# Kernel optimization log

Measured on AMD Instinct MI355X. Metric: run time of the kernel, lower is better.

Reference implementation:

```python
import jax, jax.numpy as jnp
import numpy as np

B, S, D = 16, 1024, 512
N_LAYERS = 3


def setup_inputs() -> dict:
    key = jax.random.key(0)
    ks = jax.random.split(key, 8)
    sc = 0.02  # small init scale keeps gates in a sane range
    return {
        "inputs": jax.random.normal(ks[0], (B, S, D), jnp.float32),
        "h0": jax.random.normal(ks[1], (N_LAYERS, B, D), jnp.float32),
        # GRU params, PyTorch layout: gates ordered (r, z, n), weight [3D, D]
        "w_ih": jax.random.normal(ks[2], (N_LAYERS, 3 * D, D), jnp.float32) * sc,
        "w_hh": jax.random.normal(ks[3], (N_LAYERS, 3 * D, D), jnp.float32) * sc,
        "b_ih": jnp.zeros((N_LAYERS, 3 * D), jnp.float32),
        "b_hh": jnp.zeros((N_LAYERS, 3 * D), jnp.float32),
        "ln0_g": jnp.ones((D,), jnp.float32),
        "ln0_b": jnp.zeros((D,), jnp.float32),
        "ln1_g": jnp.ones((D,), jnp.float32),
        "ln1_b": jnp.zeros((D,), jnp.float32),
        "w1": jax.random.normal(ks[4], (D, 4 * D), jnp.float32) * sc,
        "b1": jnp.zeros((4 * D,), jnp.float32),
        "w2": jax.random.normal(ks[5], (4 * D, D), jnp.float32) * sc,
        "b2": jnp.zeros((D,), jnp.float32),
    }


def _layer_norm(x, g, b, eps=1e-5):
    mu = jnp.mean(x, axis=-1, keepdims=True)
    var = jnp.var(x, axis=-1, keepdims=True)
    return (x - mu) * jax.lax.rsqrt(var + eps) * g + b


def _gru_stack(x, h0, w_ih, w_hh, b_ih, b_hh):
    # x: [S, B, D] time-major; PyTorch GRU math, gate order (r, z, n).
    for l in range(N_LAYERS):
        # precompute input projections for all timesteps (batched GEMM)
        gi = jnp.einsum('sbd,gd->sbg', x, w_ih[l]) + b_ih[l]  # [S, B, 3D]
        w_hh_l_T = w_hh[l].T
        b_hh_l = b_hh[l]

        def step(h, gi_t):
            gh = h @ w_hh_l_T + b_hh_l                       # [B, 3D]
            i_r, i_z, i_n = jnp.split(gi_t, 3, axis=-1)
            h_r, h_z, h_n = jnp.split(gh, 3, axis=-1)
            r = jax.nn.sigmoid(i_r + h_r)
            z = jax.nn.sigmoid(i_z + h_z)
            n = jnp.tanh(i_n + r * h_n)
            h_new = (1.0 - z) * n + z * h
            return h_new, h_new

        _, x = jax.lax.scan(step, h0[l], gi)                 # x: [S, B, D]
    return x


def reference(inputs, h0, w_ih, w_hh, b_ih, b_hh,
              ln0_g, ln0_b, ln1_g, ln1_b, w1, b1, w2, b2):
    # inputs: [B, S, D] -> time-major [S, B, D]
    x = _layer_norm(jnp.transpose(inputs, (1, 0, 2)), ln0_g, ln0_b)
    h = _gru_stack(x, h0, w_ih, w_hh, b_ih, b_hh)            # [S, B, D]
    out = inputs + jnp.transpose(h, (1, 0, 2))               # residual 1 (dropout=identity, eval)
    y = _layer_norm(out, ln1_g, ln1_b)
    ffn = jax.nn.gelu(y @ w1 + b1, approximate=False) @ w2 + b2
    return out + ffn                                          # residual 2
```

## Files before the change

### kernel.cpp

```cpp
#include <hip/hip_runtime.h>
#include <hip/hip_bf16.h>

typedef unsigned short u16;
typedef unsigned int   u32;
typedef unsigned long long u64;
typedef __attribute__((ext_vector_type(8))) short short8;
typedef __attribute__((ext_vector_type(4))) float f32x4;

#define WDMAX (1 << 17)

__device__ __forceinline__ float bf2f(u16 u) {
  union { u32 i; float f; } v; v.i = ((u32)u) << 16; return v.f;
}
__device__ __forceinline__ u16 f2bf(float f) {
  union { float f; u32 i; } v; v.f = f;
  return (u16)((v.i + 0x7FFFu + ((v.i >> 16) & 1u)) >> 16);
}

typedef const __attribute__((address_space(1))) u32* gas_t;
typedef __attribute__((address_space(3)))       u32* las_t;
__device__ __forceinline__ void gld16(const void* g, void* l) {
  __builtin_amdgcn_global_load_lds((gas_t)g, (las_t)l, 16, 0, 0);
}

#define WG_BARRIER() asm volatile("s_waitcnt lgkmcnt(0)\n\ts_barrier" ::: "memory")

__global__ __launch_bounds__(256) void cast_kernel(const float* __restrict__ src,
                                                   u16* __restrict__ dst, int n) {
  int i = (blockIdx.x * 256 + threadIdx.x) * 4;
  if (i >= n) return;
  float4 v = *(const float4*)(src + i);
  uint2 o;
  o.x = (u32)f2bf(v.x) | ((u32)f2bf(v.y) << 16);
  o.y = (u32)f2bf(v.z) | ((u32)f2bf(v.w) << 16);
  *(uint2*)(dst + i) = o;
}

__global__ __launch_bounds__(256) void tcast_kernel(const float* __restrict__ src,
                                                    u16* __restrict__ dst, int R, int C) {
  __shared__ u16 tile[32][33];
  int c0 = blockIdx.x * 32, r0 = blockIdx.y * 32;
  for (int dy = threadIdx.y; dy < 32; dy += 8)
    tile[dy][threadIdx.x] = f2bf(src[(size_t)(r0 + dy) * C + c0 + threadIdx.x]);
  __syncthreads();
  for (int dy = threadIdx.y; dy < 32; dy += 8)
    dst[(size_t)(c0 + dy) * R + r0 + threadIdx.x] = tile[threadIdx.x][dy];
}

__global__ __launch_bounds__(256) void hprep_kernel(const float* __restrict__ h0,
                                                    u64* __restrict__ hbuf) {
  int l = blockIdx.x;
  const float* h = h0 + l * 8192;
  u64* buf = hbuf + (size_t)l * 2 * 4096;
  for (int idx = threadIdx.x; idx < 4096; idx += 256) {
    int row = idx >> 8, wl = idx & 255;
    int d0 = wl * 2;
    u64 p0 = f2bf(h[row * 512 + d0]);
    u64 p1 = f2bf(h[row * 512 + d0 + 1]);
    buf[idx] = p0 | (p1 << 32);
  }
}

__global__ __launch_bounds__(256) void ln0_kernel(const float* __restrict__ in,
                                                  const float* __restrict__ g,
                                                  const float* __restrict__ be,
                                                  u16* __restrict__ xout) {
  int m = blockIdx.x;
  int b = m >> 10, s = m & 1023;
  int i = threadIdx.x * 2;
  float2 v = *(const float2*)(in + (size_t)m * 512 + i);
  float sum = v.x + v.y, sq = v.x * v.x + v.y * v.y;
  for (int o = 32; o > 0; o >>= 1) { sum += __shfl_down(sum, o); sq += __shfl_down(sq, o); }
  __shared__ float red[10];
  int w = threadIdx.x >> 6, lane = threadIdx.x & 63;
  if (!lane) { red[w] = sum; red[w + 4] = sq; }
  __syncthreads();
  if (threadIdx.x == 0) {
    sum = red[0] + red[1] + red[2] + red[3];
    sq  = red[4] + red[5] + red[6] + red[7];
    float mu = sum * (1.f / 512.f), var = sq * (1.f / 512.f) - mu * mu;
    red[8] = mu; red[9] = rsqrtf(var + 1e-5f);
  }
  __syncthreads();
  float mu = red[8], rs = red[9];
  u32 o0 = (u32)f2bf((v.x - mu) * rs * g[i] + be[i]) |
           ((u32)f2bf((v.y - mu) * rs * g[i + 1] + be[i + 1]) << 16);
  *(u32*)(xout + (size_t)(s * 16 + b) * 512 + i) = o0;
}

__global__ __launch_bounds__(256) void resid_ln1_kernel(const float* __restrict__ in,
                                                        const u16* __restrict__ hrec,
                                                        const float* __restrict__ g,
                                                        const float* __restrict__ be,
                                                        float* __restrict__ outf,
                                                        u16* __restrict__ y) {
  int m = blockIdx.x;
  int b = m >> 10, s = m & 1023;
  int i = threadIdx.x * 2;
  float2 v = *(const float2*)(in + (size_t)m * 512 + i);
  u32 hu = *(const u32*)(hrec + (size_t)(s * 16 + b) * 512 + i);
  v.x += bf2f((u16)(hu & 0xffff));
  v.y += bf2f((u16)(hu >> 16));
  *(float2*)(outf + (size_t)m * 512 + i) = v;
  float sum = v.x + v.y, sq = v.x * v.x + v.y * v.y;
  for (int o = 32; o > 0; o >>= 1) { sum += __shfl_down(sum, o); sq += __shfl_down(sq, o); }
  __shared__ float red[10];
  int w = threadIdx.x >> 6, lane = threadIdx.x & 63;
  if (!lane) { red[w] = sum; red[w + 4] = sq; }
  __syncthreads();
  if (threadIdx.x == 0) {
    sum = red[0] + red[1] + red[2] + red[3];
    sq  = red[4] + red[5] + red[6] + red[7];
    float mu = sum * (1.f / 512.f), var = sq * (1.f / 512.f) - mu * mu;
    red[8] = mu; red[9] = rsqrtf(var + 1e-5f);
  }
  __syncthreads();
  float mu = red[8], rs = red[9];
  u32 o0 = (u32)f2bf((v.x - mu) * rs * g[i] + be[i]) |
           ((u32)f2bf((v.y - mu) * rs * g[i + 1] + be[i + 1]) << 16);
  *(u32*)(y + (size_t)m * 512 + i) = o0;
}

template <int EPI>
__global__ __launch_bounds__(256, 2)
void gemm_bt(const u16* __restrict__ A, const u16* __restrict__ Bt,
             void* __restrict__ Out, const float* __restrict__ bias,
             const float* __restrict__ resid, int M, int N, int K) {
  __shared__ u16 As[128 * 64];
  __shared__ u16 Bs[128 * 64];
  const int bn = blockIdx.x, bm = blockIdx.y;
  const int tid = threadIdx.x;
  const int w = tid >> 6, lane = tid & 63;
  const int wr = w >> 1, wc = w & 1;
  const int col = lane & 15, kg = lane >> 4;
  const int l8 = lane >> 3, l7 = lane & 7;
  f32x4 acc[4][4];
#pragma unroll
  for (int i = 0; i < 4; ++i)
#pragma unroll
    for (int j = 0; j < 4; ++j) acc[i][j] = (f32x4){0.f, 0.f, 0.f, 0.f};

  for (int k0 = 0; k0 < K; k0 += 64) {
    __syncthreads();
#pragma unroll
    for (int i = 0; i < 4; ++i) {
      int q = w * 4 + i;
      int row = q * 8 + l8;
      int cswz = (l7 * 16) ^ ((row & 7) << 4);
      gld16((const char*)A + ((size_t)(bm * 128 + row) * K + k0) * 2 + cswz,
            (char*)As + q * 1024);
      gld16((const char*)Bt + ((size_t)(bn * 128 + row) * K + k0) * 2 + cswz,
            (char*)Bs + q * 1024);
    }
    asm volatile("s_waitcnt vmcnt(0)" ::: "memory");
    __syncthreads();
#pragma unroll
    for (int kc = 0; kc < 2; ++kc) {
      short8 af[4], bfr[4];
      int cb = kc * 64 + kg * 16;
#pragma unroll
      for (int mi = 0; mi < 4; ++mi) {
        int r = wr * 64 + mi * 16 + col;
        af[mi] = *(const short8*)((const char*)As + r * 128 + (cb ^ ((r & 7) << 4)));
      }
#pragma unroll
      for (int ni = 0; ni < 4; ++ni) {
        int r = wc * 64 + ni * 16 + col;
        bfr[ni] = *(const short8*)((const char*)Bs + r * 128 + (cb ^ ((r & 7) << 4)));
      }
#pragma unroll
      for (int mi = 0; mi < 4; ++mi)
#pragma unroll
        for (int ni = 0; ni < 4; ++ni)
          acc[mi][ni] = __builtin_amdgcn_mfma_f32_16x16x32_bf16(af[mi], bfr[ni], acc[mi][ni], 0, 0, 0);
    }
  }
#pragma unroll
  for (int ni = 0; ni < 4; ++ni) {
    int gn = bn * 128 + wc * 64 + ni * 16 + col;
    float bv = bias ? bias[gn] : 0.f;
#pragma unroll
    for (int mi = 0; mi < 4; ++mi) {
      int gmb = bm * 128 + wr * 64 + mi * 16 + kg * 4;
#pragma unroll
      for (int j = 0; j < 4; ++j) {
        float v = acc[mi][ni][j] + bv;
        size_t idx = (size_t)(gmb + j) * N + gn;
        if (EPI == 0) {
          ((u16*)Out)[idx] = f2bf(v);
        } else if (EPI == 1) {
          float gel = 0.5f * v * (1.f + erff(v * 0.7071067811865476f));
          ((u16*)Out)[idx] = f2bf(gel);
        } else {
          ((float*)Out)[idx] = v + resid[idx];
        }
      }
    }
  }
}

__device__ __forceinline__ void gather_poll(const u64* __restrict__ plane, u32 want,
                                            int w, int lane, u16* __restrict__ lds) {
  const u64 TM = 0xFFFF0000FFFF0000ULL;
  const u64 ex = ((u64)want << 16) | ((u64)want << 48);
  u64 v[16];
#pragma unroll
  for (int r = 0; r < 4; ++r)
#pragma unroll
    for (int q = 0; q < 4; ++q)
      v[r * 4 + q] = __hip_atomic_load(plane + (size_t)(w * 4 + r) * 256 + lane * 4 + q,
                                       __ATOMIC_RELAXED, __HIP_MEMORY_SCOPE_AGENT);
  for (int wd = 0; wd < WDMAX; ++wd) {
    bool ok = true;
#pragma unroll
    for (int i = 0; i < 16; ++i) ok &= ((v[i] ^ ex) & TM) == 0;
    if (ok) break;
    __builtin_amdgcn_s_sleep(1);
#pragma unroll
    for (int i = 0; i < 16; ++i)
      if (((v[i] ^ ex) & TM) != 0)
        v[i] = __hip_atomic_load(plane + (size_t)(w * 4 + (i >> 2)) * 256 + lane * 4 + (i & 3),
                                 __ATOMIC_RELAXED, __HIP_MEMORY_SCOPE_AGENT);
  }
#pragma unroll
  for (int r = 0; r < 4; ++r) {
    int row = w * 4 + r;
    uint4 pk;
    pk.x = ((u32)v[r * 4 + 0] & 0xFFFFu) | ((u32)(v[r * 4 + 0] >> 32) << 16);
    pk.y = ((u32)v[r * 4 + 1] & 0xFFFFu) | ((u32)(v[r * 4 + 1] >> 32) << 16);
    pk.z = ((u32)v[r * 4 + 2] & 0xFFFFu) | ((u32)(v[r * 4 + 2] >> 32) << 16);
    pk.w = ((u32)v[r * 4 + 3] & 0xFFFFu) | ((u32)(v[r * 4 + 3] >> 32) << 16);
    *(uint4*)((char*)lds + row * 1024 + ((lane * 16) ^ ((row & 7) << 4))) = pk;
  }
}

__global__ __launch_bounds__(256, 1)
void rec3_kernel(const u16* __restrict__ gib, const u16* __restrict__ whhb,
                 const u16* __restrict__ wihb, const float* __restrict__ bih,
                 const float* __restrict__ bhh, const float* __restrict__ h0,
                 u64* __restrict__ hpl, u64* __restrict__ xr,
                 u64* __restrict__ gip, u16* __restrict__ xout) {
  const int res = blockIdx.x & 7, grp = blockIdx.x >> 3;
  if (res > 4) return;
  __shared__ u16 hs[16 * 512];
  const int tid = threadIdx.x;
  const int w = tid >> 6, lane = tid & 63;
  const int col = lane & 15, kg = lane >> 4;
  const u64 TM = 0xFFFF0000FFFF0000ULL;

  if (res >= 3) {
    const int l = res - 2, k = grp;
    const int d = k * 64 + w * 16 + col;
    const u16* wih = wihb + (size_t)l * 1536 * 512;
    short8 wi0[16], wi1[16], wi2[16];
    {
      const u16* r0 = wih + (size_t)(0 * 512 + d) * 512;
      const u16* r1 = wih + (size_t)(1 * 512 + d) * 512;
      const u16* r2 = wih + (size_t)(2 * 512 + d) * 512;
#pragma unroll
      for (int kc = 0; kc < 16; ++kc) {
        wi0[kc] = *(const short8*)(r0 + kc * 32 + kg * 8);
        wi1[kc] = *(const short8*)(r1 + kc * 32 + kg * 8);
        wi2[kc] = *(const short8*)(r2 + kc * 32 + kg * 8);
      }
    }
    const float bi0 = bih[l * 1536 + d], bi1 = bih[l * 1536 + 512 + d],
                bi2 = bih[l * 1536 + 1024 + d];
    const u64* upx = xr + (size_t)(l - 1) * 8 * 4096;
    u64* gout = gip + (size_t)(l - 1) * 4 * 12288;
    const u64* hpc = hpl + (size_t)l * 2 * 4096;
    u64 bpv = 0;
    u64 xv[16];
    {
      const u64* pl = upx + 1 * 4096;
#pragma unroll
      for (int r = 0; r < 4; ++r)
#pragma unroll
        for (int q = 0; q < 4; ++q)
          xv[r * 4 + q] = __hip_atomic_load(pl + (size_t)(w * 4 + r) * 256 + lane * 4 + q,
                                            __ATOMIC_RELAXED, __HIP_MEMORY_SCOPE_AGENT);
    }
    for (int t = 1; t <= 1024; ++t) {
      const u64* pl = upx + (size_t)(t & 7) * 4096;
      const u64 ex = ((u64)t << 16) | ((u64)t << 48);
      for (int wd = 0; wd < WDMAX; ++wd) {
        bool ok = true;
#pragma unroll
        for (int i = 0; i < 16; ++i) ok &= ((xv[i] ^ ex) & TM) == 0;
        if (ok) break;
        __builtin_amdgcn_s_sleep(1);
#pragma unroll
        for (int r = 0; r < 4; ++r)
#pragma unroll
          for (int q = 0; q < 4; ++q)
            if (((xv[r * 4 + q] ^ ex) & TM) != 0)
              xv[r * 4 + q] = __hip_atomic_load(pl + (size_t)(w * 4 + r) * 256 + lane * 4 + q,
                                                __ATOMIC_RELAXED, __HIP_MEMORY_SCOPE_AGENT);
      }
      {
#pragma unroll
        for (int r = 0; r < 4; ++r) {
          int row = w * 4 + r;
          uint4 pk;
          pk.x = ((u32)xv[r*4+0] & 0xFFFFu) | ((u32)(xv[r*4+0] >> 32) << 16);
          pk.y = ((u32)xv[r*4+1] & 0xFFFFu) | ((u32)(xv[r*4+1] >> 32) << 16);
          pk.z = ((u32)xv[r*4+2] & 0xFFFFu) | ((u32)(xv[r*4+2] >> 32) << 16);
          pk.w = ((u32)xv[r*4+3] & 0xFFFFu) | ((u32)(xv[r*4+3] >> 32) << 16);
          *(uint4*)((char*)hs + row * 1024 + ((lane * 16) ^ ((row & 7) << 4))) = pk;
        }
      }
      WG_BARRIER();
      f32x4 ar = {0.f, 0.f, 0.f, 0.f}, az = ar, an = ar;
#pragma unroll
      for (int kc = 0; kc < 16; ++kc) {
        int cb = kc * 64 + kg * 16;
        short8 a = *(const short8*)((const char*)hs + col * 1024 + (cb ^ ((col & 7) << 4)));
        ar = __builtin_amdgcn_mfma_f32_16x16x32_bf16(a, wi0[kc], ar, 0, 0, 0);
        az = __builtin_amdgcn_mfma_f32_16x16x32_bf16(a, wi1[kc], az, 0, 0, 0);
        an = __builtin_amdgcn_mfma_f32_16x16x32_bf16(a, wi2[kc], an, 0, 0, 0);
      }
      if (t > 4) {
        u32 need = (u32)(t - 4);
        u32 ctag = (u32)(bpv >> 16) & 0xFFFFu;
        for (int wd = 0; wd < WDMAX && ctag < need; ++wd) {
          __builtin_amdgcn_s_sleep(8);
          bpv = __hip_atomic_load(hpc + (size_t)(need & 1) * 4096 + k * 32,
                                  __ATOMIC_RELAXED, __HIP_MEMORY_SCOPE_AGENT);
          ctag = (u32)(bpv >> 16) & 0xFFFFu;
        }
      }
      {
        const u32 tgl = (u32)t << 16;
        u64* slot = gout + (size_t)(t & 3) * 12288 + (size_t)k * 1536;
#pragma unroll
        for (int g = 0; g < 3; ++g) {
          f32x4 a = (g == 0) ? ar : ((g == 1) ? az : an);
          float bg = (g == 0) ? bi0 : ((g == 1) ? bi1 : bi2);
#pragma unroll
          for (int jh = 0; jh < 2; ++jh) {
            u32 lo = (u32)f2bf(a[2 * jh] + bg) | tgl;
            u32 hi = (u32)f2bf(a[2 * jh + 1] + bg) | tgl;
            __hip_atomic_store(slot + (size_t)(g * 64 + w * 16 + col) * 8 + kg * 2 + jh,
                               (u64)lo | ((u64)hi << 32),
                               __ATOMIC_RELAXED, __HIP_MEMORY_SCOPE_AGENT);
          }
        }
      }
      if (t >= 4)
        bpv = __hip_atomic_load(hpc + (size_t)((t - 3) & 1) * 4096 + k * 32,
                                __ATOMIC_RELAXED, __HIP_MEMORY_SCOPE_AGENT);
      if (t < 1024) {
        const u64* np = upx + (size_t)((t + 1) & 7) * 4096;
#pragma unroll
        for (int r = 0; r < 4; ++r)
#pragma unroll
          for (int q = 0; q < 4; ++q)
            xv[r * 4 + q] = __hip_atomic_load(np + (size_t)(w * 4 + r) * 256 + lane * 4 + q,
                                              __ATOMIC_RELAXED, __HIP_MEMORY_SCOPE_AGENT);
      }
      WG_BARRIER();
    }
    return;
  }

  const int l = res, blk = grp;
  const int d = blk * 64 + w * 16 + col;
  const u16* whh = whhb + (size_t)l * 1536 * 512;
  short8 wh0[16], wh1[16], wh2[16];
  {
    const u16* r0 = whh + (size_t)(0 * 512 + d) * 512;
    const u16* r1 = whh + (size_t)(1 * 512 + d) * 512;
    const u16* r2 = whh + (size_t)(2 * 512 + d) * 512;
#pragma unroll
    for (int kc = 0; kc < 16; ++kc) {
      wh0[kc] = *(const short8*)(r0 + kc * 32 + kg * 8);
      wh1[kc] = *(const short8*)(r1 + kc * 32 + kg * 8);
      wh2[kc] = *(const short8*)(r2 + kc * 32 + kg * 8);
    }
  }
  const float bh0 = bhh[l * 1536 + d], bh1 = bhh[l * 1536 + 512 + d],
              bh2 = bhh[l * 1536 + 1024 + d];
  float hprev[4];
#pragma unroll
  for (int j = 0; j < 4; ++j) hprev[j] = h0[l * 8192 + (kg * 4 + j) * 512 + d];

  u64* ownp = hpl + (size_t)l * 2 * 4096;
  u64* dnx = xr + (size_t)l * 8 * 4096;
  const u64* gin = gip + (size_t)(l - 1) * 4 * 12288;
  const u64* gchk = gip + (size_t)l * 4 * 12288;
  const bool ev = !(col & 1);
  u64 bp8 = 0;
  u64 gv[6] = {0, 0, 0, 0, 0, 0};

  for (int t = 1; t <= 1024; ++t) {
    float gir[3][4];
    if (l == 0) {
#pragma unroll
      for (int gte = 0; gte < 3; ++gte)
#pragma unroll
        for (int j = 0; j < 4; ++j)
          gir[gte][j] = bf2f(gib[((size_t)(t - 1) * 16 + kg * 4 + j) * 1536 + gte * 512 + d]);
    }
    gather_poll(ownp + (size_t)((t - 1) & 1) * 4096, (u32)(t - 1), w, lane, hs);
    if (l > 0) {
      const u64* gs = gin + (size_t)(t & 3) * 12288 + (size_t)blk * 1536;
      const u64 exg = ((u64)t << 16) | ((u64)t << 48);
      for (int wd = 0; wd < WDMAX; ++wd) {
        bool ok = true;
#pragma unroll
        for (int i = 0; i < 6; ++i) ok &= ((gv[i] ^ exg) & TM) == 0;
        if (ok) break;
        __builtin_amdgcn_s_sleep(1);
#pragma unroll
        for (int g = 0; g < 3; ++g)
#pragma unroll
          for (int jh = 0; jh < 2; ++jh)
            if (((gv[g * 2 + jh] ^ exg) & TM) != 0)
              gv[g * 2 + jh] = __hip_atomic_load(gs + (size_t)(g * 64 + w * 16 + col) * 8 + kg * 2 + jh,
                                                 __ATOMIC_RELAXED, __HIP_MEMORY_SCOPE_AGENT);
      }
#pragma unroll
      for (int g = 0; g < 3; ++g)
#pragma unroll
        for (int jh = 0; jh < 2; ++jh) {
          gir[g][2 * jh]     = bf2f((u16)gv[g * 2 + jh]);
          gir[g][2 * jh + 1] = bf2f((u16)(gv[g * 2 + jh] >> 32));
        }
    }
    WG_BARRIER();
    f32x4 ar = {0.f, 0.f, 0.f, 0.f}, az = ar, an = ar;
#pragma unroll
    for (int kc = 0; kc < 16; ++kc) {
      int cb = kc * 64 + kg * 16;
      short8 a = *(const short8*)((const char*)hs + col * 1024 + (cb ^ ((col & 7) << 4)));
      ar = __builtin_amdgcn_mfma_f32_16x16x32_bf16(a, wh0[kc], ar, 0, 0, 0);
      az = __builtin_amdgcn_mfma_f32_16x16x32_bf16(a, wh1[kc], az, 0, 0, 0);
      an = __builtin_amdgcn_mfma_f32_16x16x32_bf16(a, wh2[kc], an, 0, 0, 0);
    }
    u32 po[4];
#pragma unroll
    for (int j = 0; j < 4; ++j) {
      float rg = 1.f / (1.f + expf(-(gir[0][j] + ar[j] + bh0)));
      float zg = 1.f / (1.f + expf(-(gir[1][j] + az[j] + bh1)));
      float ng = tanhf(gir[2][j] + rg * (an[j] + bh2));
      float hn = (1.f - zg) * ng + zg * hprev[j];
      hprev[j] = hn;
      po[j] = (u32)f2bf(hn);
    }
    {
      const u32 tg = (u32)t << 16;
      u32 pn[4];
#pragma unroll
      for (int j = 0; j < 4; ++j) pn[j] = (u32)__shfl_xor((int)po[j], 1);
      int j0 = ev ? 0 : 2;
      u64 wd_[2]; int wi_[2];
#pragma unroll
      for (int jj = 0; jj < 2; ++jj) {
        int j = j0 + jj;
        u32 lo = (ev ? po[j] : pn[j]) | tg;
        u32 hi = (ev ? pn[j] : po[j]) | tg;
        int row = kg * 4 + j;
        wd_[jj] = (u64)lo | ((u64)hi << 32);
        wi_[jj] = row * 256 + blk * 32 + w * 8 + (col >> 1);
      }
      u64* op = ownp + (size_t)(t & 1) * 4096;
#pragma unroll
      for (int jj = 0; jj < 2; ++jj)
        __hip_atomic_store(op + wi_[jj], wd_[jj], __ATOMIC_RELAXED, __HIP_MEMORY_SCOPE_AGENT);

      if (l < 2) {
        if (t > 8) {
          u32 need = (u32)(t - 8);
          for (int wd = 0; wd < WDMAX; ++wd) {
            u32 tg8 = (lane < 8) ? (u32)((bp8 >> 16) & 0xFFFFu) : 0xFFFFu;
            if (__all(tg8 >= need)) break;
            __builtin_amdgcn_s_sleep(8);
            if (lane < 8)
              bp8 = __hip_atomic_load(gchk + (size_t)(need & 3) * 12288 + (size_t)lane * 1536,
                                      __ATOMIC_RELAXED, __HIP_MEMORY_SCOPE_AGENT);
          }
        }
        u64* xp = dnx + (size_t)(t & 7) * 4096;
#pragma unroll
        for (int jj = 0; jj < 2; ++jj)
          __hip_atomic_store(xp + wi_[jj], wd_[jj], __ATOMIC_RELAXED, __HIP_MEMORY_SCOPE_AGENT);
        if (t >= 8 && lane < 8)
          bp8 = __hip_atomic_load(gchk + (size_t)((t - 7) & 3) * 12288 + (size_t)lane * 1536,
                                  __ATOMIC_RELAXED, __HIP_MEMORY_SCOPE_AGENT);
      } else {
        u32 pr[4], qr[4];
#pragma unroll
        for (int j = 0; j < 4; ++j) {
          pr[j] = ev ? (po[j] | (pn[j] << 16)) : (pn[j] | (po[j] << 16));
          qr[j] = (u32)__shfl_xor((int)pr[j], 2);
        }
        int jx = col & 3;
        u64 raw = ((col & 2) == 0) ? ((u64)pr[jx] | ((u64)qr[jx] << 32))
                                   : ((u64)qr[jx] | ((u64)pr[jx] << 32));
        int row = kg * 4 + jx;
        *(u64*)(xout + ((size_t)(t - 1) * 16 + row) * 512 + blk * 64 + w * 16 + (col & ~3)) = raw;
      }
    }
    if (l > 0 && t < 1024) {
      const u64* gs2 = gin + (size_t)((t + 1) & 3) * 12288 + (size_t)blk * 1536;
#pragma unroll
      for (int g = 0; g < 3; ++g)
#pragma unroll
        for (int jh = 0; jh < 2; ++jh)
          gv[g * 2 + jh] = __hip_atomic_load(gs2 + (size_t)(g * 64 + w * 16 + col) * 8 + kg * 2 + jh,
                                             __ATOMIC_RELAXED, __HIP_MEMORY_SCOPE_AGENT);
    }
    WG_BARRIER();
  }
}

extern "C" void kernel_launch(void* const* d_in, const int* in_sizes, int n_in,
                              void* d_out, int out_size, void* d_ws, size_t ws_size,
                              hipStream_t stream) {
  const float* inp = (const float*)d_in[0];
  const float* h0  = (const float*)d_in[1];
  const float* wih = (const float*)d_in[2];
  const float* whh = (const float*)d_in[3];
  const float* bih = (const float*)d_in[4];
  const float* bhh = (const float*)d_in[5];
  const float* g0  = (const float*)d_in[6];
  const float* be0 = (const float*)d_in[7];
  const float* g1  = (const float*)d_in[8];
  const float* be1 = (const float*)d_in[9];
  const float* w1  = (const float*)d_in[10];
  const float* b1  = (const float*)d_in[11];
  const float* w2  = (const float*)d_in[12];
  const float* b2  = (const float*)d_in[13];
  float* out = (float*)d_out;

  char* p = (char*)d_ws;
  auto alloc = [&](size_t bytes) {
    char* r = p;
    p += (bytes + 255) & ~(size_t)255;
    return r;
  };
  u16* xa    = (u16*)alloc(16384ull * 512 * 2);
  u16* xb    = (u16*)alloc(16384ull * 512 * 2);
  u16* gib   = (u16*)alloc(16384ull * 1536 * 2);
  u16* mid   = (u16*)alloc(16384ull * 2048 * 2);
  float* outf = (float*)alloc(16384ull * 512 * 4);
  u16* wihb  = (u16*)alloc(3ull * 1536 * 512 * 2);
  u16* whhb  = (u16*)alloc(3ull * 1536 * 512 * 2);
  u16* w1t   = (u16*)alloc(2048ull * 512 * 2);
  u16* w2t   = (u16*)alloc(512ull * 2048 * 2);
  u64* hbuf  = (u64*)alloc(3ull * 2 * 4096 * 8);
  u64* xr    = (u64*)alloc(2ull * 8 * 4096 * 8);
  u64* gip   = (u64*)alloc(2ull * 4 * 12288 * 8);

  (void)hipMemsetAsync(hbuf, 0, 3ull * 2 * 4096 * 8, stream);
  (void)hipMemsetAsync(xr,   0, 2ull * 8 * 4096 * 8, stream);
  (void)hipMemsetAsync(gip,  0, 2ull * 4 * 12288 * 8, stream);
  cast_kernel<<<(3 * 1536 * 512) / 1024, 256, 0, stream>>>(wih, wihb, 3 * 1536 * 512);
  cast_kernel<<<(3 * 1536 * 512) / 1024, 256, 0, stream>>>(whh, whhb, 3 * 1536 * 512);
  hprep_kernel<<<3, 256, 0, stream>>>(h0, hbuf);
  tcast_kernel<<<dim3(2048 / 32, 512 / 32), dim3(32, 8), 0, stream>>>(w1, w1t, 512, 2048);
  tcast_kernel<<<dim3(512 / 32, 2048 / 32), dim3(32, 8), 0, stream>>>(w2, w2t, 2048, 512);
  ln0_kernel<<<16384, 256, 0, stream>>>(inp, g0, be0, xa);

  gemm_bt<0><<<dim3(12, 128), 256, 0, stream>>>(xa, wihb, (void*)gib, bih, nullptr,
                                                16384, 1536, 512);
  rec3_kernel<<<64, 256, 0, stream>>>(gib, whhb, wihb, bih, bhh, h0, hbuf, xr, gip, xb);

  resid_ln1_kernel<<<16384, 256, 0, stream>>>(inp, xb, g1, be1, outf, xa);
  gemm_bt<1><<<dim3(16, 128), 256, 0, stream>>>(xa, w1t, (void*)mid, b1, nullptr,
                                                16384, 2048, 512);
  gemm_bt<2><<<dim3(4, 128), 256, 0, stream>>>(mid, w2t, (void*)out, b2, outf,
                                               16384, 512, 2048);
}
```

Before: 4.982 ms.

## Fuse layer-0 input projection into persistent recurrence kernel with deeper ring buffers

```diff
diff --git a/kernel.cpp b/kernel.cpp
--- a/kernel.cpp
+++ b/kernel.cpp
@@ -24,6 +24,7 @@
 }
 
 #define WG_BARRIER() asm volatile("s_waitcnt lgkmcnt(0)\n\ts_barrier" ::: "memory")
+#define C_FENCE() asm volatile("" ::: "memory")
 
 __global__ __launch_bounds__(256) void cast_kernel(const float* __restrict__ src,
                                                    u16* __restrict__ dst, int n) {
@@ -186,9 +187,7 @@
       for (int j = 0; j < 4; ++j) {
         float v = acc[mi][ni][j] + bv;
         size_t idx = (size_t)(gmb + j) * N + gn;
-        if (EPI == 0) {
-          ((u16*)Out)[idx] = f2bf(v);
-        } else if (EPI == 1) {
+        if (EPI == 1) {
           float gel = 0.5f * v * (1.f + erff(v * 0.7071067811865476f));
           ((u16*)Out)[idx] = f2bf(gel);
         } else {
@@ -235,21 +234,21 @@
 }
 
 __global__ __launch_bounds__(256, 1)
-void rec3_kernel(const u16* __restrict__ gib, const u16* __restrict__ whhb,
+void rec3_kernel(const u16* __restrict__ xa, const u16* __restrict__ whhb,
                  const u16* __restrict__ wihb, const float* __restrict__ bih,
                  const float* __restrict__ bhh, const float* __restrict__ h0,
                  u64* __restrict__ hpl, u64* __restrict__ xr,
                  u64* __restrict__ gip, u16* __restrict__ xout) {
   const int res = blockIdx.x & 7, grp = blockIdx.x >> 3;
-  if (res > 4) return;
-  __shared__ u16 hs[16 * 512];
+  if (res > 5) return;
+  __shared__ u16 hs[2][16 * 512];
   const int tid = threadIdx.x;
   const int w = tid >> 6, lane = tid & 63;
   const int col = lane & 15, kg = lane >> 4;
   const u64 TM = 0xFFFF0000FFFF0000ULL;
 
   if (res >= 3) {
-    const int l = res - 2, k = grp;
+    const int l = res - 3, k = grp;
     const int d = k * 64 + w * 16 + col;
     const u16* wih = wihb + (size_t)l * 1536 * 512;
     short8 wi0[16], wi1[16], wi2[16];
@@ -266,12 +265,12 @@
     }
     const float bi0 = bih[l * 1536 + d], bi1 = bih[l * 1536 + 512 + d],
                 bi2 = bih[l * 1536 + 1024 + d];
-    const u64* upx = xr + (size_t)(l - 1) * 8 * 4096;
-    u64* gout = gip + (size_t)(l - 1) * 4 * 12288;
+    const u64* upx = (l > 0) ? (xr + (size_t)(l - 1) * 16 * 4096) : nullptr;
+    u64* gout = gip + (size_t)l * 8 * 12288;
     const u64* hpc = hpl + (size_t)l * 2 * 4096;
-    u64 bpv = 0;
+    u64 pv = 0;
     u64 xv[16];
-    {
+    if (l > 0) {
       const u64* pl = upx + 1 * 4096;
 #pragma unroll
       for (int r = 0; r < 4; ++r)
@@ -281,23 +280,33 @@
                                             __ATOMIC_RELAXED, __HIP_MEMORY_SCOPE_AGENT);
     }
     for (int t = 1; t <= 1024; ++t) {
-      const u64* pl = upx + (size_t)(t & 7) * 4096;
-      const u64 ex = ((u64)t << 16) | ((u64)t << 48);
-      for (int wd = 0; wd < WDMAX; ++wd) {
-        bool ok = true;
-#pragma unroll
-        for (int i = 0; i < 16; ++i) ok &= ((xv[i] ^ ex) & TM) == 0;
-        if (ok) break;
-        __builtin_amdgcn_s_sleep(1);
-#pragma unroll
-        for (int r = 0; r < 4; ++r)
-#pragma unroll
-          for (int q = 0; q < 4; ++q)
-            if (((xv[r * 4 + q] ^ ex) & TM) != 0)
-              xv[r * 4 + q] = __hip_atomic_load(pl + (size_t)(w * 4 + r) * 256 + lane * 4 + q,
-                                                __ATOMIC_RELAXED, __HIP_MEMORY_SCOPE_AGENT);
-      }
-      {
+      u16* hsb = hs[t & 1];
+      if (l == 0) {
+        const char* src = (const char*)(xa + (size_t)(t - 1) * 8192);
+        const u32 lo = (u32)(lane * 16);
+#pragma unroll
+        for (int r = 0; r < 4; ++r) {
+          int row = w * 4 + r;
+          *(uint4*)((char*)hsb + row * 1024 + (lo ^ (u32)((row & 7) << 4))) =
+              *(const uint4*)(src + row * 1024 + lo);
+        }
+      } else {
+        const u64* pl = upx + (size_t)(t & 15) * 4096;
+        const u64 ex = ((u64)t << 16) | ((u64)t << 48);
+        for (int wd = 0; wd < WDMAX; ++wd) {
+          bool ok = true;
+#pragma unroll
+          for (int i = 0; i < 16; ++i) ok &= ((xv[i] ^ ex) & TM) == 0;
+          if (ok) break;
+          __builtin_amdgcn_s_sleep(1);
+#pragma unroll
+          for (int r = 0; r < 4; ++r)
+#pragma unroll
+            for (int q = 0; q < 4; ++q)
+              if (((xv[r * 4 + q] ^ ex) & TM) != 0)
+                xv[r * 4 + q] = __hip_atomic_load(pl + (size_t)(w * 4 + r) * 256 + lane * 4 + q,
+                                                  __ATOMIC_RELAXED, __HIP_MEMORY_SCOPE_AGENT);
+        }
 #pragma unroll
         for (int r = 0; r < 4; ++r) {
           int row = w * 4 + r;
@@ -306,7 +315,7 @@
           pk.y = ((u32)xv[r*4+1] & 0xFFFFu) | ((u32)(xv[r*4+1] >> 32) << 16);
           pk.z = ((u32)xv[r*4+2] & 0xFFFFu) | ((u32)(xv[r*4+2] >> 32) << 16);
           pk.w = ((u32)xv[r*4+3] & 0xFFFFu) | ((u32)(xv[r*4+3] >> 32) << 16);
-          *(uint4*)((char*)hs + row * 1024 + ((lane * 16) ^ ((row & 7) << 4))) = pk;
+          *(uint4*)((char*)hsb + row * 1024 + ((lane * 16) ^ ((row & 7) << 4))) = pk;
         }
       }
       WG_BARRIER();
@@ -314,24 +323,24 @@
 #pragma unroll
       for (int kc = 0; kc < 16; ++kc) {
         int cb = kc * 64 + kg * 16;
-        short8 a = *(const short8*)((const char*)hs + col * 1024 + (cb ^ ((col & 7) << 4)));
+        short8 a = *(const short8*)((const char*)hsb + col * 1024 + (cb ^ ((col & 7) << 4)));
         ar = __builtin_amdgcn_mfma_f32_16x16x32_bf16(a, wi0[kc], ar, 0, 0, 0);
         az = __builtin_amdgcn_mfma_f32_16x16x32_bf16(a, wi1[kc], az, 0, 0, 0);
         an = __builtin_amdgcn_mfma_f32_16x16x32_bf16(a, wi2[kc], an, 0, 0, 0);
       }
-      if (t > 4) {
-        u32 need = (u32)(t - 4);
-        u32 ctag = (u32)(bpv >> 16) & 0xFFFFu;
+      if (t > 8) {
+        u32 need = (u32)(t - 8);
+        u32 ctag = (u32)(pv >> 16) & 0xFFFFu;
         for (int wd = 0; wd < WDMAX && ctag < need; ++wd) {
           __builtin_amdgcn_s_sleep(8);
-          bpv = __hip_atomic_load(hpc + (size_t)(need & 1) * 4096 + k * 32,
-                                  __ATOMIC_RELAXED, __HIP_MEMORY_SCOPE_AGENT);
-          ctag = (u32)(bpv >> 16) & 0xFFFFu;
+          pv = __hip_atomic_load(hpc + (size_t)(need & 1) * 4096 + k * 32,
+                                 __ATOMIC_RELAXED, __HIP_MEMORY_SCOPE_AGENT);
+          ctag = (u32)(pv >> 16) & 0xFFFFu;
         }
       }
       {
         const u32 tgl = (u32)t << 16;
-        u64* slot = gout + (size_t)(t & 3) * 12288 + (size_t)k * 1536;
+        u64* slot = gout + (size_t)(t & 7) * 12288 + (size_t)k * 1536;
 #pragma unroll
         for (int g = 0; g < 3; ++g) {
           f32x4 a = (g == 0) ? ar : ((g == 1) ? az : an);
@@ -346,11 +355,12 @@
           }
         }
       }
-      if (t >= 4)
-        bpv = __hip_atomic_load(hpc + (size_t)((t - 3) & 1) * 4096 + k * 32,
-                                __ATOMIC_RELAXED, __HIP_MEMORY_SCOPE_AGENT);
-      if (t < 1024) {
-        const u64* np = upx + (size_t)((t + 1) & 7) * 4096;
+      C_FENCE();
+      if (t >= 8)
+        pv = __hip_atomic_load(hpc + (size_t)((t - 7) & 1) * 4096 + k * 32,
+                               __ATOMIC_RELAXED, __HIP_MEMORY_SCOPE_AGENT);
+      if (l > 0 && t < 1024) {
+        const u64* np = upx + (size_t)((t + 1) & 15) * 4096;
 #pragma unroll
         for (int r = 0; r < 4; ++r)
 #pragma unroll
@@ -358,7 +368,6 @@
             xv[r * 4 + q] = __hip_atomic_load(np + (size_t)(w * 4 + r) * 256 + lane * 4 + q,
                                               __ATOMIC_RELAXED, __HIP_MEMORY_SCOPE_AGENT);
       }
-      WG_BARRIER();
     }
     return;
   }
@@ -385,25 +394,19 @@
   for (int j = 0; j < 4; ++j) hprev[j] = h0[l * 8192 + (kg * 4 + j) * 512 + d];
 
   u64* ownp = hpl + (size_t)l * 2 * 4096;
-  u64* dnx = xr + (size_t)l * 8 * 4096;
-  const u64* gin = gip + (size_t)(l - 1) * 4 * 12288;
-  const u64* gchk = gip + (size_t)l * 4 * 12288;
+  u64* dnx = xr + (size_t)l * 16 * 4096;
+  const u64* gin = gip + (size_t)l * 8 * 12288;
+  const u64* gchk = gip + (size_t)(l + 1) * 8 * 12288;
   const bool ev = !(col & 1);
   u64 bp8 = 0;
   u64 gv[6] = {0, 0, 0, 0, 0, 0};
 
   for (int t = 1; t <= 1024; ++t) {
+    u16* hsb = hs[t & 1];
+    gather_poll(ownp + (size_t)((t - 1) & 1) * 4096, (u32)(t - 1), w, lane, hsb);
     float gir[3][4];
-    if (l == 0) {
-#pragma unroll
-      for (int gte = 0; gte < 3; ++gte)
-#pragma unroll
-        for (int j = 0; j < 4; ++j)
-          gir[gte][j] = bf2f(gib[((size_t)(t - 1) * 16 + kg * 4 + j) * 1536 + gte * 512 + d]);
-    }
-    gather_poll(ownp + (size_t)((t - 1) & 1) * 4096, (u32)(t - 1), w, lane, hs);
-    if (l > 0) {
-      const u64* gs = gin + (size_t)(t & 3) * 12288 + (size_t)blk * 1536;
+    {
+      const u64* gs = gin + (size_t)(t & 7) * 12288 + (size_t)blk * 1536;
       const u64 exg = ((u64)t << 16) | ((u64)t << 48);
       for (int wd = 0; wd < WDMAX; ++wd) {
         bool ok = true;
@@ -432,7 +435,7 @@
 #pragma unroll
     for (int kc = 0; kc < 16; ++kc) {
       int cb = kc * 64 + kg * 16;
-      short8 a = *(const short8*)((const char*)hs + col * 1024 + (cb ^ ((col & 7) << 4)));
+      short8 a = *(const short8*)((const char*)hsb + col * 1024 + (cb ^ ((col & 7) << 4)));
       ar = __builtin_amdgcn_mfma_f32_16x16x32_bf16(a, wh0[kc], ar, 0, 0, 0);
       az = __builtin_amdgcn_mfma_f32_16x16x32_bf16(a, wh1[kc], az, 0, 0, 0);
       an = __builtin_amdgcn_mfma_f32_16x16x32_bf16(a, wh2[kc], an, 0, 0, 0);
@@ -469,23 +472,23 @@
         __hip_atomic_store(op + wi_[jj], wd_[jj], __ATOMIC_RELAXED, __HIP_MEMORY_SCOPE_AGENT);
 
       if (l < 2) {
-        if (t > 8) {
-          u32 need = (u32)(t - 8);
+        if (t > 16) {
+          u32 need = (u32)(t - 16);
           for (int wd = 0; wd < WDMAX; ++wd) {
             u32 tg8 = (lane < 8) ? (u32)((bp8 >> 16) & 0xFFFFu) : 0xFFFFu;
             if (__all(tg8 >= need)) break;
             __builtin_amdgcn_s_sleep(8);
             if (lane < 8)
-              bp8 = __hip_atomic_load(gchk + (size_t)(need & 3) * 12288 + (size_t)lane * 1536,
+              bp8 = __hip_atomic_load(gchk + (size_t)(need & 7) * 12288 + (size_t)lane * 1536,
                                       __ATOMIC_RELAXED, __HIP_MEMORY_SCOPE_AGENT);
           }
         }
-        u64* xp = dnx + (size_t)(t & 7) * 4096;
+        u64* xp = dnx + (size_t)(t & 15) * 4096;
 #pragma unroll
         for (int jj = 0; jj < 2; ++jj)
           __hip_atomic_store(xp + wi_[jj], wd_[jj], __ATOMIC_RELAXED, __HIP_MEMORY_SCOPE_AGENT);
-        if (t >= 8 && lane < 8)
-          bp8 = __hip_atomic_load(gchk + (size_t)((t - 7) & 3) * 12288 + (size_t)lane * 1536,
+        if (t >= 16 && lane < 8)
+          bp8 = __hip_atomic_load(gchk + (size_t)((t - 15) & 7) * 12288 + (size_t)lane * 1536,
                                   __ATOMIC_RELAXED, __HIP_MEMORY_SCOPE_AGENT);
       } else {
         u32 pr[4], qr[4];
@@ -501,8 +504,9 @@
         *(u64*)(xout + ((size_t)(t - 1) * 16 + row) * 512 + blk * 64 + w * 16 + (col & ~3)) = raw;
       }
     }
-    if (l > 0 && t < 1024) {
-      const u64* gs2 = gin + (size_t)((t + 1) & 3) * 12288 + (size_t)blk * 1536;
+    C_FENCE();
+    if (t < 1024) {
+      const u64* gs2 = gin + (size_t)((t + 1) & 7) * 12288 + (size_t)blk * 1536;
 #pragma unroll
       for (int g = 0; g < 3; ++g)
 #pragma unroll
@@ -510,7 +514,6 @@
           gv[g * 2 + jh] = __hip_atomic_load(gs2 + (size_t)(g * 64 + w * 16 + col) * 8 + kg * 2 + jh,
                                              __ATOMIC_RELAXED, __HIP_MEMORY_SCOPE_AGENT);
     }
-    WG_BARRIER();
   }
 }
 
@@ -541,7 +544,6 @@
   };
   u16* xa    = (u16*)alloc(16384ull * 512 * 2);
   u16* xb    = (u16*)alloc(16384ull * 512 * 2);
-  u16* gib   = (u16*)alloc(16384ull * 1536 * 2);
   u16* mid   = (u16*)alloc(16384ull * 2048 * 2);
   float* outf = (float*)alloc(16384ull * 512 * 4);
   u16* wihb  = (u16*)alloc(3ull * 1536 * 512 * 2);
@@ -549,12 +551,12 @@
   u16* w1t   = (u16*)alloc(2048ull * 512 * 2);
   u16* w2t   = (u16*)alloc(512ull * 2048 * 2);
   u64* hbuf  = (u64*)alloc(3ull * 2 * 4096 * 8);
-  u64* xr    = (u64*)alloc(2ull * 8 * 4096 * 8);
-  u64* gip   = (u64*)alloc(2ull * 4 * 12288 * 8);
+  u64* xr    = (u64*)alloc(2ull * 16 * 4096 * 8);
+  u64* gip   = (u64*)alloc(3ull * 8 * 12288 * 8);
 
   (void)hipMemsetAsync(hbuf, 0, 3ull * 2 * 4096 * 8, stream);
-  (void)hipMemsetAsync(xr,   0, 2ull * 8 * 4096 * 8, stream);
-  (void)hipMemsetAsync(gip,  0, 2ull * 4 * 12288 * 8, stream);
+  (void)hipMemsetAsync(xr,   0, 2ull * 16 * 4096 * 8, stream);
+  (void)hipMemsetAsync(gip,  0, 3ull * 8 * 12288 * 8, stream);
   cast_kernel<<<(3 * 1536 * 512) / 1024, 256, 0, stream>>>(wih, wihb, 3 * 1536 * 512);
   cast_kernel<<<(3 * 1536 * 512) / 1024, 256, 0, stream>>>(whh, whhb, 3 * 1536 * 512);
   hprep_kernel<<<3, 256, 0, stream>>>(h0, hbuf);
@@ -562,9 +564,7 @@
   tcast_kernel<<<dim3(512 / 32, 2048 / 32), dim3(32, 8), 0, stream>>>(w2, w2t, 2048, 512);
   ln0_kernel<<<16384, 256, 0, stream>>>(inp, g0, be0, xa);
 
-  gemm_bt<0><<<dim3(12, 128), 256, 0, stream>>>(xa, wihb, (void*)gib, bih, nullptr,
-                                                16384, 1536, 512);
-  rec3_kernel<<<64, 256, 0, stream>>>(gib, whhb, wihb, bih, bhh, h0, hbuf, xr, gip, xb);
+  rec3_kernel<<<64, 256, 0, stream>>>(xa, whhb, wihb, bih, bhh, h0, hbuf, xr, gip, xb);
 
   resid_ln1_kernel<<<16384, 256, 0, stream>>>(inp, xb, g1, be1, outf, xa);
   gemm_bt<1><<<dim3(16, 128), 256, 0, stream>>>(xa, w1t, (void*)mid, b1, nullptr,
```

After: 4.850 ms. -2.6%, faster.
